# Optimization experiments

Hardware: AMD Instinct MI355X
Metric: run time of the kernel (lower is better)

Reference implementation:

```python
import jax, jax.numpy as jnp
import numpy as np

EMBED_DIM = 1024
NUM_HEADS = 16
HEAD_DIM = EMBED_DIM // NUM_HEADS
SCALING = HEAD_DIM ** -0.5
NEG_FILL = -1e30


def setup_inputs() -> dict:
    key = jax.random.key(0)
    k1, k2, k3 = jax.random.split(key, 3)
    T, B, E = 2048, 4, EMBED_DIM
    query = jax.random.normal(k1, (T, B, E), dtype=jnp.float32)
    key_padding_mask = jnp.zeros((B, T), dtype=bool)  # 1 = padded key
    # xavier_uniform-like init
    lim_in = (6.0 / (3 * E + E)) ** 0.5
    in_proj_weight = jax.random.uniform(k2, (3 * E, E), minval=-lim_in, maxval=lim_in, dtype=jnp.float32)
    in_proj_bias = jnp.zeros((3 * E,), dtype=jnp.float32)
    lim_out = (6.0 / (E + E)) ** 0.5
    out_w = jax.random.uniform(k3, (E, E), minval=-lim_out, maxval=lim_out, dtype=jnp.float32)
    out_b = jnp.zeros((E,), dtype=jnp.float32)
    return {"query": query, "key_padding_mask": key_padding_mask,
            "in_proj_weight": in_proj_weight, "in_proj_bias": in_proj_bias,
            "out_w": out_w, "out_b": out_b}


def reference(query, key_padding_mask, in_proj_weight, in_proj_bias, out_w, out_b):
    T, B, E = query.shape
    H, D = NUM_HEADS, HEAD_DIM
    # fused in-projection (self-attention: qkv from same input)
    qkv = query @ in_proj_weight.T + in_proj_bias  # [T,B,3E]
    q, k, v = jnp.split(qkv, 3, axis=-1)
    q = q * SCALING
    q = q.reshape(T, B, H, D)
    k = k.reshape(T, B, H, D)
    v = v.reshape(T, B, H, D)
    # attention scores [B,H,T,S]
    scores = jnp.einsum('tbhd,sbhd->bhts', q, k)
    scores = jnp.where(key_padding_mask[:, None, None, :], NEG_FILL, scores)
    attn_w = jax.nn.softmax(scores, axis=-1)  # [B,H,T,S]
    # weighted sum of values -> [T,B,E]
    attn = jnp.einsum('bhts,sbhd->tbhd', attn_w, v).reshape(T, B, E)
    attn = attn @ out_w.T + out_b
    attn_w_avg = jnp.sum(attn_w, axis=1) / H  # [B,T,S]
    return attn, attn_w_avg
```

## Files before the change

### kernel.cpp

```cpp
#include <hip/hip_runtime.h>
#include <stdint.h>

#define QSCALE 0.18033688011112042f

typedef unsigned short u16;
typedef unsigned int u32;
typedef unsigned long long u64;
typedef __attribute__((ext_vector_type(8))) __bf16 bf16x8;
typedef __attribute__((ext_vector_type(4))) float f32x4;
typedef __attribute__((ext_vector_type(16))) float f32x16;
typedef __attribute__((ext_vector_type(8))) u16 u16x8;
typedef __attribute__((ext_vector_type(4))) u32 u32x4;

__device__ __forceinline__ void gl_lds16(const void* g, void* l) {
  __builtin_amdgcn_global_load_lds(
      (const __attribute__((address_space(1))) void*)g,
      (__attribute__((address_space(3))) void*)l, 16, 0, 0);
}

__device__ __forceinline__ u16 f2bf(float f) {
  unsigned int u = __float_as_uint(f);
  u += 0x7FFFu + ((u >> 16) & 1u);
  return (u16)(u >> 16);
}

extern "C" __global__ __launch_bounds__(256) void cvt_all(
    const float* __restrict__ query, const float* __restrict__ w_in,
    const float* __restrict__ w_out, u16* __restrict__ dst) {
  int i = (blockIdx.x * 256 + threadIdx.x) * 4;
  const float* src;
  int off;
  if (i < 8388608) {
    src = query; off = i;
  } else if (i < 11534336) {
    src = w_in; off = i - 8388608;
  } else {
    src = w_out; off = i - 11534336;
  }
  float4 v = *(const float4*)(src + off);
  ushort4 o;
  o.x = f2bf(v.x); o.y = f2bf(v.y); o.z = f2bf(v.z); o.w = f2bf(v.w);
  *(ushort4*)(dst + i) = o;
}

extern "C" __global__ __launch_bounds__(128) void mask_bits(
    const unsigned char* __restrict__ mask, u64* __restrict__ mbits) {
  const int i = threadIdx.x;
  const unsigned char* p = mask + i * 64;
  u64 bits = 0;
#pragma unroll
  for (int j = 0; j < 8; ++j) {
    const u64 c = *(const u64*)(p + j * 8);
#pragma unroll
    for (int bb = 0; bb < 8; ++bb)
      if ((c >> (8 * bb)) & 0xFFull) bits |= 1ull << (j * 8 + bb);
  }
  mbits[i] = bits;
}

extern "C" __global__ __launch_bounds__(256) void gemm_qkv(
    const u16* __restrict__ X, const u16* __restrict__ W,
    const float* __restrict__ bias,
    u16* __restrict__ qb, u16* __restrict__ kb, u16* __restrict__ vb) {
  const int tid = threadIdx.x;
  const int w = tid >> 6, lane = tid & 63;
  const int lg = lane >> 4, ll = lane & 15;
  const int wm = w >> 1, wn = w & 1;
  const int row0A = blockIdx.x * 128;
  const int row0B = blockIdx.y * 128;

  __shared__ __align__(16) u16 As[2][128 * 32];
  __shared__ __align__(16) u16 Bs[2][128 * 32];

  f32x4 acc[4][4] = {};

  const int r_st = tid >> 2;
  const int cb_st = (tid & 3) * 16;

#pragma unroll
  for (int it = 0; it < 2; ++it) {
    gl_lds16((const char*)X + ((size_t)(row0A + it * 64 + r_st) * 1024) * 2 + cb_st,
             (char*)&As[0][0] + it * 4096 + w * 1024);
    gl_lds16((const char*)W + ((size_t)(row0B + it * 64 + r_st) * 1024) * 2 + cb_st,
             (char*)&Bs[0][0] + it * 4096 + w * 1024);
  }

  for (int kt = 0; kt < 32; ++kt) {
    const int cur = kt & 1;
    asm volatile("s_waitcnt vmcnt(0)" ::: "memory");
    __syncthreads();
    if (kt + 1 < 32) {
      const int k0 = (kt + 1) * 32;
#pragma unroll
      for (int it = 0; it < 2; ++it) {
        gl_lds16((const char*)X + ((size_t)(row0A + it * 64 + r_st) * 1024 + k0) * 2 + cb_st,
                 (char*)&As[cur ^ 1][0] + it * 4096 + w * 1024);
        gl_lds16((const char*)W + ((size_t)(row0B + it * 64 + r_st) * 1024 + k0) * 2 + cb_st,
                 (char*)&Bs[cur ^ 1][0] + it * 4096 + w * 1024);
      }
    }
    const u16* Ab = &As[cur][0];
    const u16* Bb = &Bs[cur][0];
    const int kc = lg * 8;
    bf16x8 a[4], bfr[4];
#pragma unroll
    for (int i = 0; i < 4; ++i)
      a[i] = *(const bf16x8*)(Ab + (wm * 64 + i * 16 + ll) * 32 + kc);
#pragma unroll
    for (int j = 0; j < 4; ++j)
      bfr[j] = *(const bf16x8*)(Bb + (wn * 64 + j * 16 + ll) * 32 + kc);
#pragma unroll
    for (int i = 0; i < 4; ++i)
#pragma unroll
      for (int j = 0; j < 4; ++j)
        acc[i][j] = __builtin_amdgcn_mfma_f32_16x16x32_bf16(a[i], bfr[j], acc[i][j], 0, 0, 0);
  }

  const int which = row0B >> 10;
  u16* dst = which == 0 ? qb : (which == 1 ? kb : vb);
  const float scl = which == 0 ? QSCALE : 1.0f;
#pragma unroll
  for (int j = 0; j < 4; ++j) {
    const int n = row0B + wn * 64 + j * 16 + ll;
    const float bv = bias[n];
    const int n2 = n & 1023;
    const int hh = n2 >> 6, dd = n2 & 63;
#pragma unroll
    for (int i = 0; i < 4; ++i)
#pragma unroll
      for (int r = 0; r < 4; ++r) {
        const int m = row0A + wm * 64 + i * 16 + lg * 4 + r;
        const int tt = m >> 2, bb = m & 3;
        dst[((size_t)(bb * 16 + hh) * 2048 + tt) * 64 + dd] = f2bf((acc[i][j][r] + bv) * scl);
      }
  }
}

extern "C" __global__ __launch_bounds__(256) void transpose_v(
    const u16* __restrict__ v, u16* __restrict__ vt) {
  const int blk = blockIdx.x;
  const int bh = blk >> 5, tt = blk & 31;
  const int t0 = tt * 64;
  const int tid = threadIdx.x;
  __shared__ __align__(16) u16 tile[64][72];
  const u16* src = v + ((size_t)bh * 2048 + t0) * 64;
#pragma unroll
  for (int it = 0; it < 2; ++it) {
    const int r = it * 32 + (tid >> 3);
    const int c = (tid & 7) * 8;
    *(u16x8*)(&tile[r][c]) = *(const u16x8*)(src + (size_t)r * 64 + c);
  }
  __syncthreads();
  u16* dstb = vt + (size_t)bh * 64 * 2048 + t0;
#pragma unroll
  for (int it = 0; it < 2; ++it) {
    const int d = it * 32 + (tid >> 3);
    const int s = (tid & 7) * 8;
    u16x8 o;
#pragma unroll
    for (int jj = 0; jj < 8; ++jj) o[jj] = tile[s + jj][d];
    *(u16x8*)(dstb + (size_t)d * 2048 + s) = o;
  }
}

extern "C" __global__ __launch_bounds__(256, 4) void flash_fwd(
    const u16* __restrict__ q, const u16* __restrict__ k,
    const u16* __restrict__ vt, const u64* __restrict__ mbits,
    u16* __restrict__ attn_pre, float* __restrict__ stat_il) {
  const int lb = ((blockIdx.x & 7) << 7) + (blockIdx.x >> 3);
  const int bh = lb >> 4, tt = lb & 15;
  const int b = bh >> 4, hd = bh & 15;
  const int t0 = tt * 128;
  const int tid = threadIdx.x, w = tid >> 6, lane = tid & 63;
  const int hl = lane >> 5;
  const int l31 = lane & 31;

  __shared__ __align__(16) u16 Ks[3][64 * 64];
  __shared__ __align__(16) u16 Vs[2][64 * 64];

  const int qrow = t0 + w * 32 + l31;
  const u16* qp = q + ((size_t)bh * 2048 + qrow) * 64 + hl * 8;
  bf16x8 qreg[4];
#pragma unroll
  for (int kg = 0; kg < 4; ++kg) qreg[kg] = *(const bf16x8*)(qp + kg * 16);

  f32x16 po[2] = {};
  float lsum = 0.f;

  const int slot_r = tid >> 3;
  const int slot_c8 = (tid & 7) ^ (slot_r & 7);

#define STAGE_K(s_, buf_)                                                      \
  do {                                                                         \
    _Pragma("unroll") for (int it2 = 0; it2 < 2; ++it2) {                      \
      const int rr = it2 * 32 + slot_r;                                        \
      gl_lds16((const char*)k +                                                \
                   (((size_t)bh * 2048 + (s_)*64 + rr) * 64 + slot_c8 * 8) * 2,\
               (char*)&Ks[buf_][0] + it2 * 4096 + w * 1024);                   \
    }                                                                          \
  } while (0)
#define STAGE_V(s_, buf_)                                                      \
  do {                                                                         \
    _Pragma("unroll") for (int it2 = 0; it2 < 2; ++it2) {                      \
      const int rr = it2 * 32 + slot_r;                                        \
      gl_lds16((const char*)vt +                                               \
                   (((size_t)bh * 64 + rr) * 2048 + (s_)*64 + slot_c8 * 8) * 2,\
               (char*)&Vs[buf_][0] + it2 * 4096 + w * 1024);                   \
    }                                                                          \
  } while (0)

  auto QK = [&](int kbuf, int kt, f32x16& z) {
    const char* Kb = (const char*)&Ks[kbuf][0];
    f32x16 acc = {};
    const int key = kt * 32 + l31;
#pragma unroll
    for (int kg = 0; kg < 4; ++kg) {
      const bf16x8 kf = *(const bf16x8*)(
          Kb + key * 128 + ((((kg << 1) | hl) ^ (key & 7)) << 4));
      acc = __builtin_amdgcn_mfma_f32_32x32x16_bf16(kf, qreg[kg], acc, 0, 0, 0);
    }
    z = acc;
  };

  auto CONSUME = [&](int vbuf, int kt, const f32x16& z, u32 m32) {
    u32 w8[8];
#pragma unroll
    for (int h2 = 0; h2 < 2; ++h2) {
      float ps[8];
#pragma unroll
      for (int r = 0; r < 8; ++r) {
        const int ri = h2 * 8 + r;
        float p = __builtin_amdgcn_exp2f(z[ri]);
        if (m32) {
          const int bitpos = (ri & 3) + 8 * (ri >> 2) + 4 * hl;
          if ((m32 >> bitpos) & 1u) p = 0.f;
        }
        lsum += p;
        ps[r] = p;
      }
#pragma unroll
      for (int j = 0; j < 2; ++j) {
        asm("v_cvt_pk_bf16_f32 %0, %1, %2"
            : "=v"(w8[h2 * 4 + 2 * j]) : "v"(ps[4 * j]), "v"(ps[4 * j + 1]));
        asm("v_cvt_pk_bf16_f32 %0, %1, %2"
            : "=v"(w8[h2 * 4 + 2 * j + 1]) : "v"(ps[4 * j + 2]), "v"(ps[4 * j + 3]));
      }
    }
    const char* Vb = (const char*)&Vs[vbuf][0];
#pragma unroll
    for (int f = 0; f < 2; ++f) {
      u32 d0 = w8[4 * f], d1 = w8[4 * f + 1];
      u32 s0w = w8[4 * f + 2], s1w = w8[4 * f + 3];
      asm volatile("v_permlane32_swap_b32 %0, %1" : "+v"(d0), "+v"(s0w));
      asm volatile("v_permlane32_swap_b32 %0, %1" : "+v"(d1), "+v"(s1w));
      const bf16x8 pa = __builtin_bit_cast(bf16x8, (u32x4){d0, d1, s0w, s1w});
      const int g = kt * 2 + f;
      __builtin_amdgcn_s_setprio(1);
#pragma unroll
      for (int dt = 0; dt < 2; ++dt) {
        const int d = dt * 32 + l31;
        const bf16x8 vf = *(const bf16x8*)(
            Vb + d * 128 + ((((g << 1) | hl) ^ (d & 7)) << 4));
        po[dt] = __builtin_amdgcn_mfma_f32_32x32x16_bf16(pa, vf, po[dt], 0, 0, 0);
      }
      __builtin_amdgcn_s_setprio(0);
    }
  };

  STAGE_K(0, 0);
  STAGE_K(1, 1);
  STAGE_V(0, 0);
  asm volatile("s_waitcnt vmcnt(0)" ::: "memory");
  __builtin_amdgcn_s_barrier();

  f32x16 zA, zB;
  QK(0, 0, zA);

  int kb0 = 0, kb1 = 1, kb2 = 2;
  for (int t = 0; t < 32; ++t) {
    const u64 mb = mbits[b * 32 + t];
    if (t + 2 < 32) STAGE_K(t + 2, kb2);
    if (t + 1 < 32) STAGE_V(t + 1, (t + 1) & 1);

    __builtin_amdgcn_s_setprio(1);
    QK(kb0, 1, zB);
    __builtin_amdgcn_s_setprio(0);
    CONSUME(t & 1, 0, zA, (u32)mb);

    if (t < 31) {
      __builtin_amdgcn_s_setprio(1);
      QK(kb1, 0, zA);
      __builtin_amdgcn_s_setprio(0);
    }
    CONSUME(t & 1, 1, zB, (u32)(mb >> 32));

    asm volatile("s_waitcnt vmcnt(0)" ::: "memory");
    __builtin_amdgcn_s_barrier();
    const int tmp = kb0; kb0 = kb1; kb1 = kb2; kb2 = tmp;
  }

  lsum += __shfl_xor(lsum, 32, 64);
  const float linv = 1.0f / lsum;
  if (lane < 32)
    stat_il[(size_t)bh * 2048 + t0 + w * 32 + lane] = linv;

#pragma unroll
  for (int r = 0; r < 16; ++r) {
    const int qi = (r & 3) + 8 * (r >> 2) + 4 * hl;
    const float lv = __shfl(linv, qi, 64);
    const int trow = t0 + w * 32 + qi;
#pragma unroll
    for (int dt = 0; dt < 2; ++dt) {
      const int dd = dt * 32 + l31;
      attn_pre[((size_t)(trow * 4 + b)) * 1024 + hd * 64 + dd] =
          f2bf(po[dt][r] * lv);
    }
  }
#undef STAGE_K
#undef STAGE_V
}

extern "C" __global__ __launch_bounds__(256, 3) void wavg(
    const u16* __restrict__ q, const u16* __restrict__ k,
    const u64* __restrict__ mbits,
    const float* __restrict__ stat_il, float* __restrict__ wout) {
  const int lb = ((blockIdx.x & 7) << 8) + (blockIdx.x >> 3);
  const int b = lb >> 9, tt = (lb >> 5) & 15, st = lb & 31;
  const int t0 = tt * 128, s0 = st * 64;
  const int tid = threadIdx.x, w = tid >> 6, lane = tid & 63;
  const int hl = lane >> 5;
  const int l31 = lane & 31;

  __shared__ __align__(16) u16 Qs[2][128 * 64];
  __shared__ __align__(16) u16 Ks2[2][64 * 64];

  const int slot_r8 = tid >> 3;
  const int slot_c8 = (tid & 7) ^ (slot_r8 & 7);

  const u64 mbw = mbits[b * 32 + st];
  const u32 m32lo = (u32)mbw, m32hi = (u32)(mbw >> 32);
  const bool domask = mbw != 0ull;

#define STAGE_W(buf, hh)                                                       \
  do {                                                                         \
    const size_t qo_ = (size_t)(b * 16 + (hh)) * 2048;                         \
    _Pragma("unroll") for (int i2 = 0; i2 < 4; ++i2) {                         \
      const int rr = i2 * 32 + slot_r8;                                        \
      gl_lds16((const char*)q + ((qo_ + t0 + rr) * 64 + slot_c8 * 8) * 2,      \
               (char*)&Qs[buf][0] + i2 * 4096 + w * 1024);                     \
    }                                                                          \
    _Pragma("unroll") for (int i2 = 0; i2 < 2; ++i2) {                         \
      const int rr = i2 * 32 + slot_r8;                                        \
      gl_lds16((const char*)k + ((qo_ + s0 + rr) * 64 + slot_c8 * 8) * 2,      \
               (char*)&Ks2[buf][0] + i2 * 4096 + w * 1024);                    \
    }                                                                          \
  } while (0)

  STAGE_W(0, 0);
  asm volatile("s_waitcnt vmcnt(0)" ::: "memory");
  __syncthreads();

  float accw[32] = {};
  for (int h = 0; h < 16; ++h) {
    const int cur = h & 1;
    const float ilh =
        stat_il[(size_t)(b * 16 + h) * 2048 + t0 + w * 32 + l31];

    if (h + 1 < 16) STAGE_W(cur ^ 1, h + 1);

    const char* Qb = (const char*)&Qs[cur][0];
    const char* Kb = (const char*)&Ks2[cur][0];

    const int qr = w * 32 + l31;
    bf16x8 qf[4];
#pragma unroll
    for (int kg = 0; kg < 4; ++kg)
      qf[kg] = *(const bf16x8*)(
          Qb + qr * 128 + ((((kg << 1) | hl) ^ (qr & 7)) << 4));

    f32x16 z0 = {}, z1 = {};
    __builtin_amdgcn_s_setprio(1);
#pragma unroll
    for (int kg = 0; kg < 4; ++kg) {
      const int key = l31;
      const bf16x8 kf = *(const bf16x8*)(
          Kb + key * 128 + ((((kg << 1) | hl) ^ (key & 7)) << 4));
      z0 = __builtin_amdgcn_mfma_f32_32x32x16_bf16(kf, qf[kg], z0, 0, 0, 0);
    }
#pragma unroll
    for (int kg = 0; kg < 4; ++kg) {
      const int key = 32 + l31;
      const bf16x8 kf = *(const bf16x8*)(
          Kb + key * 128 + ((((kg << 1) | hl) ^ (key & 7)) << 4));
      z1 = __builtin_amdgcn_mfma_f32_32x32x16_bf16(kf, qf[kg], z1, 0, 0, 0);
    }
    __builtin_amdgcn_s_setprio(0);

#pragma unroll
    for (int r = 0; r < 16; ++r) {
      float p = __builtin_amdgcn_exp2f(z0[r]);
      if (domask) {
        const int bitpos = (r & 3) + 8 * (r >> 2) + 4 * hl;
        if ((m32lo >> bitpos) & 1u) p = 0.f;
      }
      accw[r] = fmaf(p, ilh, accw[r]);
    }
#pragma unroll
    for (int r = 0; r < 16; ++r) {
      float p = __builtin_amdgcn_exp2f(z1[r]);
      if (domask) {
        const int bitpos = (r & 3) + 8 * (r >> 2) + 4 * hl;
        if ((m32hi >> bitpos) & 1u) p = 0.f;
      }
      accw[16 + r] = fmaf(p, ilh, accw[16 + r]);
    }

    asm volatile("s_waitcnt vmcnt(0)" ::: "memory");
    __syncthreads();
  }

  float* tb = ((float*)&Qs[0][0]) + w * 2048;
#pragma unroll
  for (int kt = 0; kt < 2; ++kt)
#pragma unroll
    for (int j = 0; j < 4; ++j) {
      f32x4 qd;
#pragma unroll
      for (int e = 0; e < 4; ++e) qd[e] = accw[kt * 16 + 4 * j + e] * 0.0625f;
      const int slot = kt * 8 + 2 * j + hl;
      *(f32x4*)(tb + l31 * 64 + ((slot ^ (l31 & 7)) << 2)) = qd;
    }
  __syncthreads();
#pragma unroll
  for (int j2 = 0; j2 < 8; ++j2) {
    const int row = j2 * 4 + (lane >> 4);
    const int slot = lane & 15;
    const f32x4 v = *(const f32x4*)(tb + row * 64 + ((slot ^ (row & 7)) << 2));
    *(f32x4*)(wout + ((size_t)b * 2048 + t0 + w * 32 + row) * 2048 + s0 +
              slot * 4) = v;
  }
#undef STAGE_W
}

extern "C" __global__ __launch_bounds__(256) void gemm_out(
    const u16* __restrict__ A, const u16* __restrict__ W,
    const float* __restrict__ bias, float* __restrict__ out) {
  const int tid = threadIdx.x;
  const int w = tid >> 6, lane = tid & 63;
  const int lg = lane >> 4, ll = lane & 15;
  const int wm = w >> 1, wn = w & 1;
  const int row0A = blockIdx.x * 128;
  const int row0B = blockIdx.y * 128;

  __shared__ __align__(16) u16 As[2][128 * 32];
  __shared__ __align__(16) u16 Bs[2][128 * 32];

  f32x4 acc[4][4] = {};
  const int r_st = tid >> 2;
  const int cb_st = (tid & 3) * 16;

#pragma unroll
  for (int it = 0; it < 2; ++it) {
    gl_lds16((const char*)A + ((size_t)(row0A + it * 64 + r_st) * 1024) * 2 + cb_st,
             (char*)&As[0][0] + it * 4096 + w * 1024);
    gl_lds16((const char*)W + ((size_t)(row0B + it * 64 + r_st) * 1024) * 2 + cb_st,
             (char*)&Bs[0][0] + it * 4096 + w * 1024);
  }

  for (int kt = 0; kt < 32; ++kt) {
    const int cur = kt & 1;
    asm volatile("s_waitcnt vmcnt(0)" ::: "memory");
    __syncthreads();
    if (kt + 1 < 32) {
      const int k0 = (kt + 1) * 32;
#pragma unroll
      for (int it = 0; it < 2; ++it) {
        gl_lds16((const char*)A + ((size_t)(row0A + it * 64 + r_st) * 1024 + k0) * 2 + cb_st,
                 (char*)&As[cur ^ 1][0] + it * 4096 + w * 1024);
        gl_lds16((const char*)W + ((size_t)(row0B + it * 64 + r_st) * 1024 + k0) * 2 + cb_st,
                 (char*)&Bs[cur ^ 1][0] + it * 4096 + w * 1024);
      }
    }
    const u16* Ab = &As[cur][0];
    const u16* Bb = &Bs[cur][0];
    const int kc = lg * 8;
    bf16x8 a[4], bfr[4];
#pragma unroll
    for (int i = 0; i < 4; ++i)
      a[i] = *(const bf16x8*)(Ab + (wm * 64 + i * 16 + ll) * 32 + kc);
#pragma unroll
    for (int j = 0; j < 4; ++j)
      bfr[j] = *(const bf16x8*)(Bb + (wn * 64 + j * 16 + ll) * 32 + kc);
#pragma unroll
    for (int i = 0; i < 4; ++i)
#pragma unroll
      for (int j = 0; j < 4; ++j)
        acc[i][j] = __builtin_amdgcn_mfma_f32_16x16x32_bf16(a[i], bfr[j], acc[i][j], 0, 0, 0);
  }

#pragma unroll
  for (int j = 0; j < 4; ++j) {
    const int n = row0B + wn * 64 + j * 16 + ll;
    const float bv = bias[n];
#pragma unroll
    for (int i = 0; i < 4; ++i)
#pragma unroll
      for (int r = 0; r < 4; ++r) {
        const int m = row0A + wm * 64 + i * 16 + lg * 4 + r;
        out[(size_t)m * 1024 + n] = acc[i][j][r] + bv;
      }
  }
}

extern "C" void kernel_launch(void* const* d_in, const int* in_sizes, int n_in,
                              void* d_out, int out_size, void* d_ws, size_t ws_size,
                              hipStream_t stream) {
  const float* query = (const float*)d_in[0];
  const unsigned char* mask = (const unsigned char*)d_in[1];
  const float* w_in = (const float*)d_in[2];
  const float* b_in = (const float*)d_in[3];
  const float* w_out = (const float*)d_in[4];
  const float* b_out = (const float*)d_in[5];

  float* out0 = (float*)d_out;
  float* outw = out0 + (size_t)8388608;

  char* ws = (char*)d_ws;
  u16* Xbf   = (u16*)(ws + 0);
  u16* Wqkv  = (u16*)(ws + 16777216);
  u16* Woutb = (u16*)(ws + 23068672);
  u16* qb    = (u16*)(ws + 25165824);
  u16* kb    = (u16*)(ws + 41943040);
  u16* vb    = (u16*)(ws + 58720256);
  u16* vtb   = (u16*)(ws + 75497472);
  u16* ap    = (u16*)(ws + 92274688);
  float* sil = (float*)(ws + 109051904);
  u64* mbits = (u64*)(ws + 109576192);

  cvt_all<<<12288, 256, 0, stream>>>(query, w_in, w_out, Xbf);
  mask_bits<<<1, 128, 0, stream>>>(mask, mbits);
  gemm_qkv<<<dim3(64, 24), 256, 0, stream>>>(Xbf, Wqkv, b_in, qb, kb, vb);
  transpose_v<<<2048, 256, 0, stream>>>(vb, vtb);
  flash_fwd<<<1024, 256, 0, stream>>>(qb, kb, vtb, mbits, ap, sil);
  wavg<<<2048, 256, 0, stream>>>(qb, kb, mbits, sil, outw);
  gemm_out<<<dim3(64, 8), 256, 0, stream>>>(ap, Woutb, b_out, out0);
}
```

Measured before the change: 289.9 us.

## Triple-buffer GEMM loads, simplify flash loop, and switch PV path to fp16

Both projection GEMMs move from a double-buffered loop with a full wait each step to a three-stage ring buffer that keeps one tile load in flight, so global-to-LDS latency overlaps the MFMA work. The V projection is now stored as fp16 instead of bf16. The flash kernel drops its software-pipelined QK/consume interleave and uses a simpler two-buffer loop that loads K and V together. In that loop the probabilities are packed to fp16 with cvt_pkrtz, row sums are accumulated with fdot2, and P·V runs on fp16 MFMA. This trades flash-loop overlap for fewer instructions and more fp16 mantissa precision, with some risk that removing the pipelining exposes load latency.

```diff
diff --git a/kernel.cpp b/kernel.cpp
--- a/kernel.cpp
+++ b/kernel.cpp
@@ -6,6 +6,9 @@
 typedef unsigned short u16;
 typedef unsigned int u32;
 typedef unsigned long long u64;
+typedef _Float16 f16;
+typedef __attribute__((ext_vector_type(2))) __fp16 h16x2;
+typedef __attribute__((ext_vector_type(8))) _Float16 f16x8;
 typedef __attribute__((ext_vector_type(8))) __bf16 bf16x8;
 typedef __attribute__((ext_vector_type(4))) float f32x4;
 typedef __attribute__((ext_vector_type(16))) float f32x16;
@@ -69,38 +72,37 @@
   const int row0A = blockIdx.x * 128;
   const int row0B = blockIdx.y * 128;
 
-  __shared__ __align__(16) u16 As[2][128 * 32];
-  __shared__ __align__(16) u16 Bs[2][128 * 32];
+  __shared__ __align__(16) u16 As[3][128 * 32];
+  __shared__ __align__(16) u16 Bs[3][128 * 32];
 
   f32x4 acc[4][4] = {};
 
   const int r_st = tid >> 2;
   const int cb_st = (tid & 3) * 16;
 
-#pragma unroll
-  for (int it = 0; it < 2; ++it) {
-    gl_lds16((const char*)X + ((size_t)(row0A + it * 64 + r_st) * 1024) * 2 + cb_st,
-             (char*)&As[0][0] + it * 4096 + w * 1024);
-    gl_lds16((const char*)W + ((size_t)(row0B + it * 64 + r_st) * 1024) * 2 + cb_st,
-             (char*)&Bs[0][0] + it * 4096 + w * 1024);
-  }
-
+#define STAGE_G(s_, buf_)                                                      \
+  do {                                                                         \
+    const int k0_ = (s_) * 32;                                                 \
+    _Pragma("unroll") for (int it2 = 0; it2 < 2; ++it2) {                      \
+      gl_lds16((const char*)X +                                                \
+                   ((size_t)(row0A + it2 * 64 + r_st) * 1024 + k0_) * 2 + cb_st,\
+               (char*)&As[buf_][0] + it2 * 4096 + w * 1024);                   \
+      gl_lds16((const char*)W +                                                \
+                   ((size_t)(row0B + it2 * 64 + r_st) * 1024 + k0_) * 2 + cb_st,\
+               (char*)&Bs[buf_][0] + it2 * 4096 + w * 1024);                   \
+    }                                                                          \
+  } while (0)
+
+  STAGE_G(0, 0);
+  STAGE_G(1, 1);
+  asm volatile("s_waitcnt vmcnt(4)" ::: "memory");
+  __builtin_amdgcn_s_barrier();
+
+  int c0 = 0, c1 = 1, c2 = 2;
   for (int kt = 0; kt < 32; ++kt) {
-    const int cur = kt & 1;
-    asm volatile("s_waitcnt vmcnt(0)" ::: "memory");
-    __syncthreads();
-    if (kt + 1 < 32) {
-      const int k0 = (kt + 1) * 32;
-#pragma unroll
-      for (int it = 0; it < 2; ++it) {
-        gl_lds16((const char*)X + ((size_t)(row0A + it * 64 + r_st) * 1024 + k0) * 2 + cb_st,
-                 (char*)&As[cur ^ 1][0] + it * 4096 + w * 1024);
-        gl_lds16((const char*)W + ((size_t)(row0B + it * 64 + r_st) * 1024 + k0) * 2 + cb_st,
-                 (char*)&Bs[cur ^ 1][0] + it * 4096 + w * 1024);
-      }
-    }
-    const u16* Ab = &As[cur][0];
-    const u16* Bb = &Bs[cur][0];
+    if (kt + 2 < 32) STAGE_G(kt + 2, c2);
+    const u16* Ab = &As[c0][0];
+    const u16* Bb = &Bs[c0][0];
     const int kc = lg * 8;
     bf16x8 a[4], bfr[4];
 #pragma unroll
@@ -114,25 +116,53 @@
 #pragma unroll
       for (int j = 0; j < 4; ++j)
         acc[i][j] = __builtin_amdgcn_mfma_f32_16x16x32_bf16(a[i], bfr[j], acc[i][j], 0, 0, 0);
-  }
+    if (kt + 2 < 32)
+      asm volatile("s_waitcnt vmcnt(4)" ::: "memory");
+    else
+      asm volatile("s_waitcnt vmcnt(0)" ::: "memory");
+    __builtin_amdgcn_s_barrier();
+    const int tmp = c0; c0 = c1; c1 = c2; c2 = tmp;
+  }
+#undef STAGE_G
 
   const int which = row0B >> 10;
-  u16* dst = which == 0 ? qb : (which == 1 ? kb : vb);
-  const float scl = which == 0 ? QSCALE : 1.0f;
-#pragma unroll
-  for (int j = 0; j < 4; ++j) {
-    const int n = row0B + wn * 64 + j * 16 + ll;
-    const float bv = bias[n];
-    const int n2 = n & 1023;
-    const int hh = n2 >> 6, dd = n2 & 63;
-#pragma unroll
-    for (int i = 0; i < 4; ++i)
-#pragma unroll
-      for (int r = 0; r < 4; ++r) {
-        const int m = row0A + wm * 64 + i * 16 + lg * 4 + r;
-        const int tt = m >> 2, bb = m & 3;
-        dst[((size_t)(bb * 16 + hh) * 2048 + tt) * 64 + dd] = f2bf((acc[i][j][r] + bv) * scl);
-      }
+  if (which == 2) {
+#pragma unroll
+    for (int j = 0; j < 4; ++j) {
+      const int n = row0B + wn * 64 + j * 16 + ll;
+      const float bv = bias[n];
+      const int n2 = n & 1023;
+      const int hh = n2 >> 6, dd = n2 & 63;
+#pragma unroll
+      for (int i = 0; i < 4; ++i)
+#pragma unroll
+        for (int r = 0; r < 4; ++r) {
+          const int m = row0A + wm * 64 + i * 16 + lg * 4 + r;
+          const int tt = m >> 2, bb = m & 3;
+          const f16 hv = (f16)(acc[i][j][r] + bv);
+          vb[((size_t)(bb * 16 + hh) * 2048 + tt) * 64 + dd] =
+              __builtin_bit_cast(u16, hv);
+        }
+    }
+  } else {
+    u16* dst = which == 0 ? qb : kb;
+    const float scl = which == 0 ? QSCALE : 1.0f;
+#pragma unroll
+    for (int j = 0; j < 4; ++j) {
+      const int n = row0B + wn * 64 + j * 16 + ll;
+      const float bv = bias[n];
+      const int n2 = n & 1023;
+      const int hh = n2 >> 6, dd = n2 & 63;
+#pragma unroll
+      for (int i = 0; i < 4; ++i)
+#pragma unroll
+        for (int r = 0; r < 4; ++r) {
+          const int m = row0A + wm * 64 + i * 16 + lg * 4 + r;
+          const int tt = m >> 2, bb = m & 3;
+          dst[((size_t)(bb * 16 + hh) * 2048 + tt) * 64 + dd] =
+              f2bf((acc[i][j][r] + bv) * scl);
+        }
+    }
   }
 }
 
@@ -175,7 +205,7 @@
   const int hl = lane >> 5;
   const int l31 = lane & 31;
 
-  __shared__ __align__(16) u16 Ks[3][64 * 64];
+  __shared__ __align__(16) u16 Ks[2][64 * 64];
   __shared__ __align__(16) u16 Vs[2][64 * 64];
 
   const int qrow = t0 + w * 32 + l31;
@@ -185,120 +215,98 @@
   for (int kg = 0; kg < 4; ++kg) qreg[kg] = *(const bf16x8*)(qp + kg * 16);
 
   f32x16 po[2] = {};
-  float lsum = 0.f;
+  float ls0 = 0.f, ls1 = 0.f;
+  const h16x2 ones = {(__fp16)1.0f, (__fp16)1.0f};
 
   const int slot_r = tid >> 3;
   const int slot_c8 = (tid & 7) ^ (slot_r & 7);
 
-#define STAGE_K(s_, buf_)                                                      \
+#define STAGE_F(buf, s0_)                                                      \
   do {                                                                         \
     _Pragma("unroll") for (int it2 = 0; it2 < 2; ++it2) {                      \
       const int rr = it2 * 32 + slot_r;                                        \
       gl_lds16((const char*)k +                                                \
-                   (((size_t)bh * 2048 + (s_)*64 + rr) * 64 + slot_c8 * 8) * 2,\
-               (char*)&Ks[buf_][0] + it2 * 4096 + w * 1024);                   \
+                   (((size_t)bh * 2048 + (s0_) + rr) * 64 + slot_c8 * 8) * 2,  \
+               (char*)&Ks[buf][0] + it2 * 4096 + w * 1024);                    \
+      gl_lds16((const char*)vt +                                               \
+                   (((size_t)bh * 64 + rr) * 2048 + (s0_) + slot_c8 * 8) * 2,  \
+               (char*)&Vs[buf][0] + it2 * 4096 + w * 1024);                    \
     }                                                                          \
   } while (0)
-#define STAGE_V(s_, buf_)                                                      \
-  do {                                                                         \
-    _Pragma("unroll") for (int it2 = 0; it2 < 2; ++it2) {                      \
-      const int rr = it2 * 32 + slot_r;                                        \
-      gl_lds16((const char*)vt +                                               \
-                   (((size_t)bh * 64 + rr) * 2048 + (s_)*64 + slot_c8 * 8) * 2,\
-               (char*)&Vs[buf_][0] + it2 * 4096 + w * 1024);                   \
-    }                                                                          \
-  } while (0)
-
-  auto QK = [&](int kbuf, int kt, f32x16& z) {
-    const char* Kb = (const char*)&Ks[kbuf][0];
-    f32x16 acc = {};
-    const int key = kt * 32 + l31;
-#pragma unroll
-    for (int kg = 0; kg < 4; ++kg) {
-      const bf16x8 kf = *(const bf16x8*)(
-          Kb + key * 128 + ((((kg << 1) | hl) ^ (key & 7)) << 4));
-      acc = __builtin_amdgcn_mfma_f32_32x32x16_bf16(kf, qreg[kg], acc, 0, 0, 0);
-    }
-    z = acc;
-  };
-
-  auto CONSUME = [&](int vbuf, int kt, const f32x16& z, u32 m32) {
-    u32 w8[8];
-#pragma unroll
-    for (int h2 = 0; h2 < 2; ++h2) {
-      float ps[8];
-#pragma unroll
-      for (int r = 0; r < 8; ++r) {
-        const int ri = h2 * 8 + r;
-        float p = __builtin_amdgcn_exp2f(z[ri]);
-        if (m32) {
-          const int bitpos = (ri & 3) + 8 * (ri >> 2) + 4 * hl;
-          if ((m32 >> bitpos) & 1u) p = 0.f;
-        }
-        lsum += p;
-        ps[r] = p;
-      }
-#pragma unroll
-      for (int j = 0; j < 2; ++j) {
-        asm("v_cvt_pk_bf16_f32 %0, %1, %2"
-            : "=v"(w8[h2 * 4 + 2 * j]) : "v"(ps[4 * j]), "v"(ps[4 * j + 1]));
-        asm("v_cvt_pk_bf16_f32 %0, %1, %2"
-            : "=v"(w8[h2 * 4 + 2 * j + 1]) : "v"(ps[4 * j + 2]), "v"(ps[4 * j + 3]));
-      }
-    }
-    const char* Vb = (const char*)&Vs[vbuf][0];
-#pragma unroll
-    for (int f = 0; f < 2; ++f) {
-      u32 d0 = w8[4 * f], d1 = w8[4 * f + 1];
-      u32 s0w = w8[4 * f + 2], s1w = w8[4 * f + 3];
-      asm volatile("v_permlane32_swap_b32 %0, %1" : "+v"(d0), "+v"(s0w));
-      asm volatile("v_permlane32_swap_b32 %0, %1" : "+v"(d1), "+v"(s1w));
-      const bf16x8 pa = __builtin_bit_cast(bf16x8, (u32x4){d0, d1, s0w, s1w});
-      const int g = kt * 2 + f;
-      __builtin_amdgcn_s_setprio(1);
-#pragma unroll
-      for (int dt = 0; dt < 2; ++dt) {
-        const int d = dt * 32 + l31;
-        const bf16x8 vf = *(const bf16x8*)(
-            Vb + d * 128 + ((((g << 1) | hl) ^ (d & 7)) << 4));
-        po[dt] = __builtin_amdgcn_mfma_f32_32x32x16_bf16(pa, vf, po[dt], 0, 0, 0);
-      }
-      __builtin_amdgcn_s_setprio(0);
-    }
-  };
-
-  STAGE_K(0, 0);
-  STAGE_K(1, 1);
-  STAGE_V(0, 0);
+
+  STAGE_F(0, 0);
   asm volatile("s_waitcnt vmcnt(0)" ::: "memory");
   __builtin_amdgcn_s_barrier();
 
-  f32x16 zA, zB;
-  QK(0, 0, zA);
-
-  int kb0 = 0, kb1 = 1, kb2 = 2;
   for (int t = 0; t < 32; ++t) {
     const u64 mb = mbits[b * 32 + t];
-    if (t + 2 < 32) STAGE_K(t + 2, kb2);
-    if (t + 1 < 32) STAGE_V(t + 1, (t + 1) & 1);
-
-    __builtin_amdgcn_s_setprio(1);
-    QK(kb0, 1, zB);
-    __builtin_amdgcn_s_setprio(0);
-    CONSUME(t & 1, 0, zA, (u32)mb);
-
-    if (t < 31) {
+    const int cur = t & 1;
+    if (t + 1 < 32) STAGE_F(cur ^ 1, (t + 1) * 64);
+
+    const char* Kb = (const char*)&Ks[cur][0];
+    const char* Vb = (const char*)&Vs[cur][0];
+
+#pragma unroll
+    for (int kt = 0; kt < 2; ++kt) {
+      f32x16 z = {};
+      const int key = kt * 32 + l31;
       __builtin_amdgcn_s_setprio(1);
-      QK(kb1, 0, zA);
+#pragma unroll
+      for (int kg = 0; kg < 4; ++kg) {
+        const bf16x8 kf = *(const bf16x8*)(
+            Kb + key * 128 + ((((kg << 1) | hl) ^ (key & 7)) << 4));
+        z = __builtin_amdgcn_mfma_f32_32x32x16_bf16(kf, qreg[kg], z, 0, 0, 0);
+      }
       __builtin_amdgcn_s_setprio(0);
-    }
-    CONSUME(t & 1, 1, zB, (u32)(mb >> 32));
+
+      float ps[16];
+#pragma unroll
+      for (int r = 0; r < 16; ++r) ps[r] = __builtin_amdgcn_exp2f(z[r]);
+      const u32 m32 = (u32)(mb >> (kt * 32));
+      if (m32) {
+#pragma unroll
+        for (int r = 0; r < 16; ++r) {
+          const int bitpos = (r & 3) + 8 * (r >> 2) + 4 * hl;
+          if ((m32 >> bitpos) & 1u) ps[r] = 0.f;
+        }
+      }
+
+      u32 w8[8];
+#pragma unroll
+      for (int j = 0; j < 8; ++j) {
+        const h16x2 pk = __builtin_amdgcn_cvt_pkrtz(ps[2 * j], ps[2 * j + 1]);
+        w8[j] = __builtin_bit_cast(u32, pk);
+        if (j & 1)
+          ls1 = __builtin_amdgcn_fdot2(pk, ones, ls1, false);
+        else
+          ls0 = __builtin_amdgcn_fdot2(pk, ones, ls0, false);
+      }
+
+#pragma unroll
+      for (int f = 0; f < 2; ++f) {
+        u32 d0 = w8[4 * f], d1 = w8[4 * f + 1];
+        u32 s0w = w8[4 * f + 2], s1w = w8[4 * f + 3];
+        asm volatile("v_permlane32_swap_b32 %0, %1" : "+v"(d0), "+v"(s0w));
+        asm volatile("v_permlane32_swap_b32 %0, %1" : "+v"(d1), "+v"(s1w));
+        const f16x8 pa = __builtin_bit_cast(f16x8, (u32x4){d0, d1, s0w, s1w});
+        const int g = kt * 2 + f;
+        __builtin_amdgcn_s_setprio(1);
+#pragma unroll
+        for (int dt = 0; dt < 2; ++dt) {
+          const int d = dt * 32 + l31;
+          const f16x8 vf = *(const f16x8*)(
+              Vb + d * 128 + ((((g << 1) | hl) ^ (d & 7)) << 4));
+          po[dt] = __builtin_amdgcn_mfma_f32_32x32x16_f16(pa, vf, po[dt], 0, 0, 0);
+        }
+        __builtin_amdgcn_s_setprio(0);
+      }
+    }
 
     asm volatile("s_waitcnt vmcnt(0)" ::: "memory");
     __builtin_amdgcn_s_barrier();
-    const int tmp = kb0; kb0 = kb1; kb1 = kb2; kb2 = tmp;
-  }
-
+  }
+
+  float lsum = ls0 + ls1;
   lsum += __shfl_xor(lsum, 32, 64);
   const float linv = 1.0f / lsum;
   if (lane < 32)
@@ -316,8 +324,7 @@
           f2bf(po[dt][r] * lv);
     }
   }
-#undef STAGE_K
-#undef STAGE_V
+#undef STAGE_F
 }
 
 extern "C" __global__ __launch_bounds__(256, 3) void wavg(
@@ -452,37 +459,36 @@
   const int row0A = blockIdx.x * 128;
   const int row0B = blockIdx.y * 128;
 
-  __shared__ __align__(16) u16 As[2][128 * 32];
-  __shared__ __align__(16) u16 Bs[2][128 * 32];
+  __shared__ __align__(16) u16 As[3][128 * 32];
+  __shared__ __align__(16) u16 Bs[3][128 * 32];
 
   f32x4 acc[4][4] = {};
   const int r_st = tid >> 2;
   const int cb_st = (tid & 3) * 16;
 
-#pragma unroll
-  for (int it = 0; it < 2; ++it) {
-    gl_lds16((const char*)A + ((size_t)(row0A + it * 64 + r_st) * 1024) * 2 + cb_st,
-             (char*)&As[0][0] + it * 4096 + w * 1024);
-    gl_lds16((const char*)W + ((size_t)(row0B + it * 64 + r_st) * 1024) * 2 + cb_st,
-             (char*)&Bs[0][0] + it * 4096 + w * 1024);
-  }
-
+#define STAGE_G(s_, buf_)                                                      \
+  do {                                                                         \
+    const int k0_ = (s_) * 32;                                                 \
+    _Pragma("unroll") for (int it2 = 0; it2 < 2; ++it2) {                      \
+      gl_lds16((const char*)A +                                                \
+                   ((size_t)(row0A + it2 * 64 + r_st) * 1024 + k0_) * 2 + cb_st,\
+               (char*)&As[buf_][0] + it2 * 4096 + w * 1024);                   \
+      gl_lds16((const char*)W +                                                \
+                   ((size_t)(row0B + it2 * 64 + r_st) * 1024 + k0_) * 2 + cb_st,\
+               (char*)&Bs[buf_][0] + it2 * 4096 + w * 1024);                   \
+    }                                                                          \
+  } while (0)
+
+  STAGE_G(0, 0);
+  STAGE_G(1, 1);
+  asm volatile("s_waitcnt vmcnt(4)" ::: "memory");
+  __builtin_amdgcn_s_barrier();
+
+  int c0 = 0, c1 = 1, c2 = 2;
   for (int kt = 0; kt < 32; ++kt) {
-    const int cur = kt & 1;
-    asm volatile("s_waitcnt vmcnt(0)" ::: "memory");
-    __syncthreads();
-    if (kt + 1 < 32) {
-      const int k0 = (kt + 1) * 32;
-#pragma unroll
-      for (int it = 0; it < 2; ++it) {
-        gl_lds16((const char*)A + ((size_t)(row0A + it * 64 + r_st) * 1024 + k0) * 2 + cb_st,
-                 (char*)&As[cur ^ 1][0] + it * 4096 + w * 1024);
-        gl_lds16((const char*)W + ((size_t)(row0B + it * 64 + r_st) * 1024 + k0) * 2 + cb_st,
-                 (char*)&Bs[cur ^ 1][0] + it * 4096 + w * 1024);
-      }
-    }
-    const u16* Ab = &As[cur][0];
-    const u16* Bb = &Bs[cur][0];
+    if (kt + 2 < 32) STAGE_G(kt + 2, c2);
+    const u16* Ab = &As[c0][0];
+    const u16* Bb = &Bs[c0][0];
     const int kc = lg * 8;
     bf16x8 a[4], bfr[4];
 #pragma unroll
@@ -496,7 +502,14 @@
 #pragma unroll
       for (int j = 0; j < 4; ++j)
         acc[i][j] = __builtin_amdgcn_mfma_f32_16x16x32_bf16(a[i], bfr[j], acc[i][j], 0, 0, 0);
-  }
+    if (kt + 2 < 32)
+      asm volatile("s_waitcnt vmcnt(4)" ::: "memory");
+    else
+      asm volatile("s_waitcnt vmcnt(0)" ::: "memory");
+    __builtin_amdgcn_s_barrier();
+    const int tmp = c0; c0 = c1; c1 = c2; c2 = tmp;
+  }
+#undef STAGE_G
 
 #pragma unroll
   for (int j = 0; j < 4; ++j) {
```

Result: faster. 280.2 us (-3.4%).
